# Performance work log

Hardware: AMD Instinct MI355X
Metric: run time of the kernel (lower is better)

## Reference

```python
import jax, jax.numpy as jnp
import numpy as np

N = 10000      # nodes
E = 100000     # edges
D = 768        # hidden = heads * head_dim
H = 4          # heads
C = D // H     # 192 per-head channels
EDIM = 16      # edge feature dim
NREL = 10      # num relations
L = 3          # num TransformerConv layers


def setup_inputs() -> dict:
    key = jax.random.key(0)
    ks = jax.random.split(key, 16)
    s = 0.02
    x = jax.random.normal(ks[0], (N, D), jnp.float32)
    edge_index = jax.random.randint(ks[1], (2, E), 0, N, jnp.int32)
    rel = jax.random.randint(ks[2], (E,), 0, NREL).astype(jnp.float32)
    w = jax.random.uniform(ks[3], (E,), jnp.float32)
    edge_attr = jnp.stack([rel, w], axis=1)  # [E, 2]: (relation_id, weight)
    rel_emb = jax.random.normal(ks[4], (NREL, EDIM - 1), jnp.float32) * s
    W_edge = jax.random.normal(ks[5], (EDIM, EDIM), jnp.float32) * s
    b_edge = jnp.zeros((EDIM,), jnp.float32)
    Wk = jax.random.normal(ks[6], (L, D, D), jnp.float32) * s
    bk = jnp.zeros((L, D), jnp.float32)
    Wq = jax.random.normal(ks[7], (L, D, D), jnp.float32) * s
    bq = jnp.zeros((L, D), jnp.float32)
    Wv = jax.random.normal(ks[8], (L, D, D), jnp.float32) * s
    bv = jnp.zeros((L, D), jnp.float32)
    We = jax.random.normal(ks[9], (L, EDIM, D), jnp.float32) * s   # lin_edge, no bias (PyG)
    Wskip = jax.random.normal(ks[10], (L, D, D), jnp.float32) * s  # root/skip linear
    bskip = jnp.zeros((L, D), jnp.float32)
    ln_g = jnp.ones((D,), jnp.float32)
    ln_b = jnp.zeros((D,), jnp.float32)
    return dict(x=x, edge_attr=edge_attr, edge_index=edge_index, rel_emb=rel_emb,
                W_edge=W_edge, b_edge=b_edge, Wk=Wk, bk=bk, Wq=Wq, bq=bq,
                Wv=Wv, bv=bv, We=We, Wskip=Wskip, bskip=bskip, ln_g=ln_g, ln_b=ln_b)


def reference(x, edge_attr, edge_index, rel_emb, W_edge, b_edge,
              Wk, bk, Wq, bq, Wv, bv, We, Wskip, bskip, ln_g, ln_b):
    src, dst = edge_index[0], edge_index[1]
    # _process_edge_features: embed relation id, concat weight, project
    rel_ids = jnp.clip(jax.lax.stop_gradient(edge_attr[:, 0]).astype(jnp.int32), 0, NREL - 1)
    ef = jnp.concatenate([rel_emb[rel_ids], edge_attr[:, 1:2]], axis=-1) @ W_edge + b_edge  # [E,16]
    scale = 1.0 / np.sqrt(C)
    h = x  # input_proj is Identity (input_dim == hidden_dim)
    for l in range(L):
        q = (h @ Wq[l] + bq[l]).reshape(N, H, C)
        k = (h @ Wk[l] + bk[l]).reshape(N, H, C)
        v = (h @ Wv[l] + bv[l]).reshape(N, H, C)
        e = (ef @ We[l]).reshape(E, H, C)           # per-edge embedding
        kj = k[src] + e                              # [E,H,C]
        alpha = jnp.einsum('ehc,ehc->eh', q[dst], kj) * scale  # [E,H]
        # scatter-softmax over incoming edges of each destination node
        m = jax.ops.segment_max(jax.lax.stop_gradient(alpha), dst, num_segments=N)
        a = jnp.exp(alpha - m[dst])
        denom = jax.ops.segment_sum(a, dst, num_segments=N)
        a = a / (denom[dst] + 1e-16)
        msg = (v[src] + e) * a[..., None]            # [E,H,C]
        out = jax.ops.segment_sum(msg.reshape(E, H * C), dst, num_segments=N)
        h = out + h @ Wskip[l] + bskip[l]            # root_weight skip connection
        if l < L - 1:
            h = jax.nn.gelu(h, approximate=False)    # dropout: eval mode -> identity
    mu = jnp.mean(h, axis=-1, keepdims=True)
    var = jnp.mean((h - mu) ** 2, axis=-1, keepdims=True)
    h = (h - mu) / jnp.sqrt(var + 1e-5) * ln_g + ln_b
    return jnp.mean(h, axis=0)  # global_mean_pool over single graph -> [D]
```

## Files before the change

### kernel.cpp

```cpp
#include <hip/hip_runtime.h>
#include <hip/hip_bf16.h>
#include <math.h>
#include <stdint.h>

#define NN 10000
#define EE 100000
#define DD 768
#define HH 4
#define CC 192
#define EDIM 16
#define NREL 10
#define MP 10240
#define NQ2 3200
#define NB 3136
#define SCALE 0.07216878364870322f

using short8  = __attribute__((ext_vector_type(8))) short;
using floatx4 = __attribute__((ext_vector_type(4))) float;


__device__ __forceinline__ float b2f(short u) {
    union { unsigned int i; float f; } t;
    t.i = ((unsigned int)(unsigned short)u) << 16;
    return t.f;
}

__device__ __forceinline__ short f2b(float f) {
    __hip_bfloat16 h = __float2bfloat16(f);
    short r;
    __builtin_memcpy(&r, &h, 2);
    return r;
}

__device__ __forceinline__ __hip_bfloat16 rd_any(const void* p, long long j, int bf) {
    if (bf) return ((const __hip_bfloat16*)p)[j];
    return __float2bfloat16(((const float*)p)[j]);
}

__device__ __forceinline__ void gload16(const __hip_bfloat16* g, __hip_bfloat16* l) {
    __builtin_amdgcn_global_load_lds(
        (const __attribute__((address_space(1))) unsigned int*)g,
        (__attribute__((address_space(3))) unsigned int*)l, 16, 0, 0);
}

__global__ __launch_bounds__(256) void detect_zero(const void* edge_attr,
                                                   int* flag, int* counts) {
    int i = blockIdx.x * 256 + threadIdx.x;
    if (i < NN) counts[i] = 0;
    if (blockIdx.x == 0 && threadIdx.x < 64) {
        const unsigned short* p = (const unsigned short*)edge_attr;
        int nz = (p[4 * threadIdx.x] != 0) ? 1 : 0;
        unsigned long long m = __ballot(nz);
        if (threadIdx.x == 0) *flag = (__popcll(m) > 8) ? 1 : 0;
    }
}


__global__ __launch_bounds__(256) void cvt_big(
    const void* x, const void* We, const int* flag,
    __hip_bfloat16* hb, __hip_bfloat16* Web) {
    long long i = (long long)blockIdx.x * 256 + threadIdx.x;
    int bf = *flag;
    const long long NX = (long long)NN * DD;
    const long long NE2 = 3LL * EDIM * DD;
    if (i < NX) { hb[i] = rd_any(x, i, bf); return; } i -= NX;
    if (i < NE2) { Web[i] = rd_any(We, i, bf); return; } i -= NE2;
    if (i < (long long)(MP - NN) * DD) hb[(long long)NN * DD + i] = __float2bfloat16(0.0f);
}

__global__ __launch_bounds__(256) void cvt_small(
    const void* ea, const void* rel, const void* Wed, const void* bed,
    const void* bk, const void* bq, const void* bv, const void* bs,
    const void* lg, const void* lb, const int* flag,
    __hip_bfloat16* eab, __hip_bfloat16* relb, __hip_bfloat16* Wedb,
    __hip_bfloat16* bedb, __hip_bfloat16* ballb, __hip_bfloat16* lgb,
    __hip_bfloat16* lbb) {
    long long i = (long long)blockIdx.x * 256 + threadIdx.x;
    int bf = *flag;
    if (i < 2LL * EE) { eab[i] = rd_any(ea, i, bf); return; } i -= 2LL * EE;
    if (i < NREL * (EDIM - 1)) { relb[i] = rd_any(rel, i, bf); return; } i -= NREL * (EDIM - 1);
    if (i < EDIM * EDIM) { Wedb[i] = rd_any(Wed, i, bf); return; } i -= EDIM * EDIM;
    if (i < EDIM) { bedb[i] = rd_any(bed, i, bf); return; } i -= EDIM;
    if (i < 3 * NB) {
        int l = (int)(i / NB), c = (int)(i % NB);
        const void* src; long long off;
        if (c < 768)       { src = bq; off = (long long)l * DD + c; }
        else if (c < 1536) { src = bk; off = (long long)l * DD + (c - 768); }
        else if (c < 2304) { src = bv; off = (long long)l * DD + (c - 1536); }
        else if (c < 3072) { src = bs; off = (long long)l * DD + (c - 2304); }
        else { ballb[i] = __float2bfloat16(0.0f); return; }
        ballb[i] = rd_any(src, off, bf); return;
    } i -= 3 * NB;
    if (i < DD) { lgb[i] = rd_any(lg, i, bf); return; } i -= DD;
    if (i < DD) { lbb[i] = rd_any(lb, i, bf); return; }
}

__global__ __launch_bounds__(256) void wt_all(
    const void* Wq, const void* Wk, const void* Wv, const void* Ws,
    const int* flag, __hip_bfloat16* Wt3) {
    __shared__ __hip_bfloat16 tile[32][33];
    int mm = blockIdx.y;
    int l = mm >> 2, m = mm & 3;
    const void* src = (m == 0) ? Wq : (m == 1) ? Wk : (m == 2) ? Wv : Ws;
    int bx = blockIdx.x;
    int tr = bx / 24, tc = bx % 24;
    int k0 = tr * 32, c0 = tc * 32;
    int t = threadIdx.x;
    int rr = t >> 5, cc = t & 31;
    int bf = *flag;
    long long base = (long long)l * DD * DD;
#pragma unroll
    for (int p = 0; p < 4; p++)
        tile[p * 8 + rr][cc] =
            rd_any(src, base + (long long)(k0 + p * 8 + rr) * DD + c0 + cc, bf);
    __syncthreads();
    __hip_bfloat16* dst = Wt3 + (size_t)l * NB * DD + (size_t)(m * 768 + c0) * DD + k0;
#pragma unroll
    for (int p = 0; p < 4; p++)
        dst[(size_t)(p * 8 + rr) * DD + cc] = tile[cc][p * 8 + rr];
}

__global__ __launch_bounds__(256) void mq_kernel(
    const void* Wq, const void* bq, const int* flag,
    const __hip_bfloat16* __restrict__ Web, __hip_bfloat16* __restrict__ Wt3,
    __hip_bfloat16* __restrict__ ballb) {
    __shared__ float WeS[16][193];
    const int lh = blockIdx.y, l = lh >> 2, hh = lh & 3;
    const int t = threadIdx.x;
    const int bf = *flag;
    for (int i = t; i < 16 * 192; i += 256) {
        int j = i / 192, c = i % 192;
        WeS[j][c] = (float)Web[(size_t)l * EDIM * DD + (size_t)j * DD + hh * CC + c];
    }
    __syncthreads();
    const int k = blockIdx.x * 64 + (t >> 2);
    const int j0 = (t & 3) * 4;
    float s0 = 0.f, s1 = 0.f, s2 = 0.f, s3 = 0.f;
    if (bf) {
        const short8* qp = (const short8*)((const __hip_bfloat16*)Wq +
            ((size_t)l * DD + k) * DD + hh * CC);
#pragma unroll 4
        for (int ch = 0; ch < 24; ch++) {
            short8 v = qp[ch];
#pragma unroll
            for (int u = 0; u < 8; u++) {
                float w = b2f(v[u]);
                int c = ch * 8 + u;
                s0 += w * WeS[j0 + 0][c]; s1 += w * WeS[j0 + 1][c];
                s2 += w * WeS[j0 + 2][c]; s3 += w * WeS[j0 + 3][c];
            }
        }
    } else {
        const float4* qp = (const float4*)((const float*)Wq +
            ((size_t)l * DD + k) * DD + hh * CC);
#pragma unroll 4
        for (int ch = 0; ch < 48; ch++) {
            float4 v = qp[ch];
            float wv[4] = {v.x, v.y, v.z, v.w};
#pragma unroll
            for (int u = 0; u < 4; u++) {
                float w = wv[u];
                int c = ch * 4 + u;
                s0 += w * WeS[j0 + 0][c]; s1 += w * WeS[j0 + 1][c];
                s2 += w * WeS[j0 + 2][c]; s3 += w * WeS[j0 + 3][c];
            }
        }
    }
    const size_t base = (size_t)l * NB * DD;
    const int row = 3072 + hh * 16 + j0;
    Wt3[base + (size_t)(row + 0) * DD + k] = __float2bfloat16(s0);
    Wt3[base + (size_t)(row + 1) * DD + k] = __float2bfloat16(s1);
    Wt3[base + (size_t)(row + 2) * DD + k] = __float2bfloat16(s2);
    Wt3[base + (size_t)(row + 3) * DD + k] = __float2bfloat16(s3);
    if (blockIdx.x == 0 && t < 4) {
        float b0 = 0.f, b1 = 0.f, b2 = 0.f, b3 = 0.f;
        for (int c = 0; c < CC; c++) {
            float w = (float)rd_any(bq, (long long)l * DD + hh * CC + c, bf);
            b0 += w * WeS[j0 + 0][c]; b1 += w * WeS[j0 + 1][c];
            b2 += w * WeS[j0 + 2][c]; b3 += w * WeS[j0 + 3][c];
        }
        ballb[l * NB + 3072 + hh * 16 + j0 + 0] = __float2bfloat16(b0);
        ballb[l * NB + 3072 + hh * 16 + j0 + 1] = __float2bfloat16(b1);
        ballb[l * NB + 3072 + hh * 16 + j0 + 2] = __float2bfloat16(b2);
        ballb[l * NB + 3072 + hh * 16 + j0 + 3] = __float2bfloat16(b3);
    }
}


__global__ __launch_bounds__(256) void count_kernel(const int* ei, int* counts) {
    int e = blockIdx.x * 256 + threadIdx.x;
    if (e < EE) atomicAdd(&counts[ei[EE + e]], 1);
}

__global__ __launch_bounds__(256) void scan_kernel(const int* counts, int* rowptr,
                                                   int* cursor) {
    __shared__ int sdata[256];
    int t = threadIdx.x;
    int base = t * 40;
    int cnt = (base < NN) ? min(40, NN - base) : 0;
    int s = 0;
    for (int i = 0; i < cnt; i++) s += counts[base + i];
    sdata[t] = s;
    __syncthreads();
    for (int off = 1; off < 256; off <<= 1) {
        int add = (t >= off) ? sdata[t - off] : 0;
        __syncthreads();
        sdata[t] += add;
        __syncthreads();
    }
    int run = sdata[t] - s;
    for (int i = 0; i < cnt; i++) {
        cursor[base + i] = run;
        run += counts[base + i];
        rowptr[base + i + 1] = run;
    }
    if (t == 0) rowptr[0] = 0;
}

__global__ __launch_bounds__(256) void fill_kernel(const int* ei, int* cursor,
                                                   int* eids, int* esrc) {
    int e = blockIdx.x * 256 + threadIdx.x;
    if (e < EE) {
        int d = ei[EE + e];
        int pos = atomicAdd(&cursor[d], 1);
        eids[pos] = e;
        esrc[pos] = ei[e];
    }
}


__global__ __launch_bounds__(256) void ef_kernel(
    const int* __restrict__ eids,
    const __hip_bfloat16* __restrict__ eab, const __hip_bfloat16* __restrict__ relb,
    const __hip_bfloat16* __restrict__ Wedb, const __hip_bfloat16* __restrict__ bedb,
    __hip_bfloat16* __restrict__ efb) {
    int idx = blockIdx.x * 256 + threadIdx.x;
    if (idx >= EE * EDIM) return;
    int p = idx >> 4, j = idx & 15;
    int e = eids[p];
    int rid = (int)((float)eab[e * 2 + 0]);
    rid = min(max(rid, 0), NREL - 1);
    float w = (float)eab[e * 2 + 1];
    float s = (float)bedb[j];
#pragma unroll
    for (int i = 0; i < 15; i++)
        s += (float)relb[rid * 15 + i] * (float)Wedb[i * EDIM + j];
    s += w * (float)Wedb[15 * EDIM + j];
    efb[idx] = __float2bfloat16(s);
}


__device__ __forceinline__ void stage_half(const __hip_bfloat16* g, int row0, int ktile,
                                           char* ldsdst, int tid) {
#pragma unroll
    for (int j = 0; j < 2; ++j) {
        int c = j * 512 + tid;
        int row = c >> 3;
        int sch = (c & 7) ^ (row & 7);
        gload16(g + (size_t)(row0 + row) * DD + ktile * 64 + sch * 8,
                (__hip_bfloat16*)(ldsdst + c * 16));
    }
}

#define MF16(va, vb, cc) cc = __builtin_amdgcn_mfma_f32_16x16x32_bf16(va, vb, cc, 0, 0, 0)
#define BAR() __builtin_amdgcn_s_barrier()
#define WLG() asm volatile("s_waitcnt lgkmcnt(0)" ::: "memory")
#define WVM(N) asm volatile("s_waitcnt vmcnt(" #N ")" ::: "memory")
#define SB() __builtin_amdgcn_sched_barrier(0)
#define LDS8(off) (*(const short8*)(smem + (off)))

__global__ __launch_bounds__(512) void gemm256(
    const __hip_bfloat16* __restrict__ A, const __hip_bfloat16* __restrict__ Bt,
    const __hip_bfloat16* __restrict__ bias, __hip_bfloat16* __restrict__ C) {
    __shared__ __align__(16) char smem[131072];
    const int bid = (int)blockIdx.x;
    const int tid = threadIdx.x;
    const int wid = tid >> 6, lane = tid & 63;
    const int quad = lane >> 4, l15 = lane & 15;

    if (bid >= 480) {
        const int qb = bid - 480;
        const int m0q = qb * 64;
        const __hip_bfloat16* Bq = Bt + (size_t)3072 * DD;
        const int xq0 = (quad ^ (l15 & 7)) * 16;
        const int xq1 = ((quad + 4) ^ (l15 & 7)) * 16;
        floatx4 qacc[4] = {};
        for (int kt = 0; kt < 12; ++kt) {
#pragma unroll
            for (int j = 0; j < 2; ++j) {
                int c = j * 512 + tid;
                int hf = c >> 9;
                int cc = c & 511;
                int row = cc >> 3;
                int sch = (cc & 7) ^ (row & 7);
                const __hip_bfloat16* src = hf
                    ? (Bq + (size_t)row * DD + kt * 64 + sch * 8)
                    : (A + (size_t)(m0q + row) * DD + kt * 64 + sch * 8);
                gload16(src, (__hip_bfloat16*)(smem + c * 16));
            }
            asm volatile("s_waitcnt vmcnt(0)" ::: "memory");
            BAR();
            if (wid < 4) {
                short8 a0 = LDS8((wid * 16 + l15) * 128 + xq0);
                short8 a1 = LDS8((wid * 16 + l15) * 128 + xq1);
#pragma unroll
                for (int nt = 0; nt < 4; ++nt) {
                    short8 b0 = LDS8(8192 + (nt * 16 + l15) * 128 + xq0);
                    short8 b1 = LDS8(8192 + (nt * 16 + l15) * 128 + xq1);
                    MF16(a0, b0, qacc[nt]);
                    MF16(a1, b1, qacc[nt]);
                }
            }
            WLG();
            BAR();
        }
        if (wid < 4) {
#pragma unroll
            for (int nt = 0; nt < 4; ++nt) {
                float bb = (float)bias[3072 + nt * 16 + l15];
#pragma unroll
                for (int r = 0; r < 4; ++r) {
                    int row = m0q + wid * 16 + quad * 4 + r;
                    if (row < NN)
                        C[(size_t)row * NQ2 + 3072 + nt * 16 + l15] =
                            __float2bfloat16(qacc[nt][r] + bb);
                }
            }
        }
        return;
    }

    const int wm = wid >> 2, wn = wid & 3;
    const int swz = (bid & 7) * 60 + (bid >> 3);
    const int m0 = (swz / 12) * 256;
    const int n0 = (swz % 12) * 256;

    const int xa0 = (quad ^ (l15 & 7)) * 16;
    const int xa1 = ((quad + 4) ^ (l15 & 7)) * 16;
    const int aRow = (wm * 128 + l15) * 128;
    const int bRow = 32768 + (wn * 64 + l15) * 128;

    floatx4 acc[8][4] = {};
    short8 a[4][2], bA[2][2], bB[2][2];

    stage_half(A, m0, 0, smem + 0, tid);
    stage_half(A, m0 + 128, 0, smem + 16384, tid);
    stage_half(Bt, n0, 0, smem + 32768, tid);
    stage_half(Bt, n0 + 128, 0, smem + 49152, tid);
    stage_half(Bt, n0, 1, smem + 98304, tid);
    stage_half(Bt, n0 + 128, 1, smem + 114688, tid);
    WVM(4);
    BAR();

#pragma unroll 1
    for (int it = 0; it < 6; ++it) {
        const int kA = 2 * it + 1;
        const int kB = (it < 5) ? 2 * it + 2 : 0;
        const int kC = (it < 5) ? 2 * it + 3 : 1;
        stage_half(A, m0, kA, smem + 65536, tid);
        stage_half(A, m0 + 128, kA, smem + 81920, tid);
#pragma unroll
        for (int mt = 0; mt < 4; ++mt) {
            a[mt][0] = LDS8(aRow + mt * 2048 + xa0);
            a[mt][1] = LDS8(aRow + mt * 2048 + xa1);
        }
#pragma unroll
        for (int nt = 0; nt < 2; ++nt) {
            bA[nt][0] = LDS8(bRow + nt * 2048 + xa0);
            bA[nt][1] = LDS8(bRow + nt * 2048 + xa1);
            bB[nt][0] = LDS8(bRow + (nt + 2) * 2048 + xa0);
            bB[nt][1] = LDS8(bRow + (nt + 2) * 2048 + xa1);
        }
        SB(); BAR(); WLG(); SB();
        __builtin_amdgcn_s_setprio(1);
#pragma unroll
        for (int mt = 0; mt < 4; ++mt)
#pragma unroll
            for (int nt = 0; nt < 2; ++nt) {
                MF16(a[mt][0], bA[nt][0], acc[mt][nt]);
                MF16(a[mt][1], bA[nt][1], acc[mt][nt]);
                MF16(a[mt][0], bB[nt][0], acc[mt][nt + 2]);
                MF16(a[mt][1], bB[nt][1], acc[mt][nt + 2]);
            }
        __builtin_amdgcn_s_setprio(0);
        stage_half(Bt, n0, kB, smem + 32768, tid);
        stage_half(Bt, n0 + 128, kB, smem + 49152, tid);
#pragma unroll
        for (int mt = 0; mt < 4; ++mt) {
            a[mt][0] = LDS8(aRow + (mt + 4) * 2048 + xa0);
            a[mt][1] = LDS8(aRow + (mt + 4) * 2048 + xa1);
        }
        WVM(4);
        SB(); BAR(); WLG(); SB();
        __builtin_amdgcn_s_setprio(1);
#pragma unroll
        for (int mt = 0; mt < 4; ++mt)
#pragma unroll
            for (int nt = 0; nt < 2; ++nt) {
                MF16(a[mt][0], bB[nt][0], acc[mt + 4][nt + 2]);
                MF16(a[mt][1], bB[nt][1], acc[mt + 4][nt + 2]);
                MF16(a[mt][0], bA[nt][0], acc[mt + 4][nt]);
                MF16(a[mt][1], bA[nt][1], acc[mt + 4][nt]);
            }
        __builtin_amdgcn_s_setprio(0);
        stage_half(A, m0, kB, smem + 0, tid);
        stage_half(A, m0 + 128, kB, smem + 16384, tid);
#pragma unroll
        for (int mt = 0; mt < 4; ++mt) {
            a[mt][0] = LDS8(65536 + aRow + mt * 2048 + xa0);
            a[mt][1] = LDS8(65536 + aRow + mt * 2048 + xa1);
        }
#pragma unroll
        for (int nt = 0; nt < 2; ++nt) {
            bA[nt][0] = LDS8(65536 + bRow + nt * 2048 + xa0);
            bA[nt][1] = LDS8(65536 + bRow + nt * 2048 + xa1);
            bB[nt][0] = LDS8(65536 + bRow + (nt + 2) * 2048 + xa0);
            bB[nt][1] = LDS8(65536 + bRow + (nt + 2) * 2048 + xa1);
        }
        SB(); BAR(); WLG(); SB();
        __builtin_amdgcn_s_setprio(1);
#pragma unroll
        for (int mt = 0; mt < 4; ++mt)
#pragma unroll
            for (int nt = 0; nt < 2; ++nt) {
                MF16(a[mt][0], bA[nt][0], acc[mt][nt]);
                MF16(a[mt][1], bA[nt][1], acc[mt][nt]);
                MF16(a[mt][0], bB[nt][0], acc[mt][nt + 2]);
                MF16(a[mt][1], bB[nt][1], acc[mt][nt + 2]);
            }
        __builtin_amdgcn_s_setprio(0);
        stage_half(Bt, n0, kC, smem + 98304, tid);
        stage_half(Bt, n0 + 128, kC, smem + 114688, tid);
#pragma unroll
        for (int mt = 0; mt < 4; ++mt) {
            a[mt][0] = LDS8(65536 + aRow + (mt + 4) * 2048 + xa0);
            a[mt][1] = LDS8(65536 + aRow + (mt + 4) * 2048 + xa1);
        }
        WVM(4);
        SB(); BAR(); WLG(); SB();
        __builtin_amdgcn_s_setprio(1);
#pragma unroll
        for (int mt = 0; mt < 4; ++mt)
#pragma unroll
            for (int nt = 0; nt < 2; ++nt) {
                MF16(a[mt][0], bB[nt][0], acc[mt + 4][nt + 2]);
                MF16(a[mt][1], bB[nt][1], acc[mt + 4][nt + 2]);
                MF16(a[mt][0], bA[nt][0], acc[mt + 4][nt]);
                MF16(a[mt][1], bA[nt][1], acc[mt + 4][nt]);
            }
        __builtin_amdgcn_s_setprio(0);
    }

    asm volatile("s_waitcnt vmcnt(0)" ::: "memory");
    BAR();
    {
        short* stg = (short*)smem + wid * 1152;
        float bv[4];
#pragma unroll
        for (int nt = 0; nt < 4; ++nt)
            bv[nt] = (float)bias[n0 + wn * 64 + nt * 16 + l15];
        const int rdo = (lane >> 2) * 68 + (lane & 3) * 16;
        const int grow0 = m0 + wm * 128 + (lane >> 2);
        const int gcol = n0 + wn * 64 + (lane & 3) * 16;
#pragma unroll
        for (int mt = 0; mt < 8; ++mt) {
#pragma unroll
            for (int nt = 0; nt < 4; ++nt)
#pragma unroll
                for (int r = 0; r < 4; ++r)
                    stg[(quad * 4 + r) * 68 + nt * 16 + l15] =
                        f2b(acc[mt][nt][r] + bv[nt]);
            asm volatile("s_waitcnt lgkmcnt(0)" ::: "memory");
            short8 v0 = *(const short8*)(stg + rdo);
            short8 v1 = *(const short8*)(stg + rdo + 8);
            int grow = grow0 + mt * 16;
            if (grow < NN) {
                short8* dp = (short8*)(C + (size_t)grow * NQ2 + gcol);
                dp[0] = v0; dp[1] = v1;
            }
            asm volatile("s_waitcnt lgkmcnt(0)" ::: "memory");
        }
    }
}


__global__ __launch_bounds__(256) void node_attn(
    const int* __restrict__ rowptr, const int* __restrict__ esrc,
    const __hip_bfloat16* __restrict__ qkvs, const __hip_bfloat16* __restrict__ efb,
    const __hip_bfloat16* __restrict__ Wel, __hip_bfloat16* __restrict__ hb,
    int do_gelu) {
    const int wv = threadIdx.x >> 6, lane = threadIdx.x & 63;
    const int n = blockIdx.x * 2 + (wv >> 1);
    const int half = wv & 1;
    const int cb = half * 384 + lane * 6;
    const int sj = lane & 15;
    const int hsel = lane & 32;
    const float qe_gate = ((lane & 16) == 0) ? 1.0f : 0.0f;
    const int s0 = rowptr[n], s1 = rowptr[n + 1];
    const short* qk = (const short*)qkvs;
    float q[6];
    {
        const short2* qp = (const short2*)(qk + (size_t)n * NQ2 + cb);
        short2 a = qp[0], b = qp[1], c = qp[2];
        q[0] = b2f(a.x) * SCALE; q[1] = b2f(a.y) * SCALE; q[2] = b2f(b.x) * SCALE;
        q[3] = b2f(b.y) * SCALE; q[4] = b2f(c.x) * SCALE; q[5] = b2f(c.y) * SCALE;
    }
    const float qe_l = b2f(qk[(size_t)n * NQ2 + 3072 + (half * 2 + (lane >> 5)) * 16 + sj])
                       * SCALE * qe_gate;
    float m = -INFINITY, lsum = 0.f, sacc = 0.f;
    float acc[6] = {};
    short2 ka = {0,0}, kb = {0,0}, kc = {0,0};
    short2 va = {0,0}, vb = {0,0}, vc = {0,0};
    float efv = 0.f;
    if (s0 < s1) {
        int src = esrc[s0];
        const short2* kp = (const short2*)(qk + (size_t)src * NQ2 + 768 + cb);
        const short2* vp = (const short2*)(qk + (size_t)src * NQ2 + 1536 + cb);
        ka = kp[0]; kb = kp[1]; kc = kp[2];
        va = vp[0]; vb = vp[1]; vc = vp[2];
        efv = b2f(((const short*)efb)[(size_t)s0 * 16 + sj]);
    }
    for (int p = s0; p < s1; p++) {
        short2 nka = ka, nkb = kb, nkc = kc, nva = va, nvb = vb, nvc = vc;
        float nefv = efv;
        if (p + 1 < s1) {
            int src = esrc[p + 1];
            const short2* kp = (const short2*)(qk + (size_t)src * NQ2 + 768 + cb);
            const short2* vp = (const short2*)(qk + (size_t)src * NQ2 + 1536 + cb);
            nka = kp[0]; nkb = kp[1]; nkc = kp[2];
            nva = vp[0]; nvb = vp[1]; nvc = vp[2];
            nefv = b2f(((const short*)efb)[(size_t)(p + 1) * 16 + sj]);
        }
        float part = qe_l * efv;
        part += q[0] * b2f(ka.x) + q[1] * b2f(ka.y) + q[2] * b2f(kb.x);
        part += q[3] * b2f(kb.y) + q[4] * b2f(kc.x) + q[5] * b2f(kc.y);
        part += __shfl_xor(part, 1); part += __shfl_xor(part, 2);
        part += __shfl_xor(part, 4); part += __shfl_xor(part, 8);
        part += __shfl_xor(part, 16);
        if (part > m + 8.0f) {
            float sc = __expf(m - part);
            m = part;
            lsum *= sc; sacc *= sc;
#pragma unroll
            for (int i = 0; i < 6; i++) acc[i] *= sc;
        }
        float w = __expf(part - m);
        lsum += w;
        sacc += w * efv;
        acc[0] += w * b2f(va.x); acc[1] += w * b2f(va.y);
        acc[2] += w * b2f(vb.x); acc[3] += w * b2f(vb.y);
        acc[4] += w * b2f(vc.x); acc[5] += w * b2f(vc.y);
        ka = nka; kb = nkb; kc = nkc; va = nva; vb = nvb; vc = nvc; efv = nefv;
    }
    float inv = 1.0f / (lsum + 1e-16f);
#pragma unroll
    for (int i = 0; i < 6; i++) acc[i] *= inv;
    float sS = sacc * inv;
    {
        const short2* sp = (const short2*)(qk + (size_t)n * NQ2 + 2304 + cb);
        short2 a = sp[0], b = sp[1], c = sp[2];
        acc[0] += b2f(a.x); acc[1] += b2f(a.y); acc[2] += b2f(b.x);
        acc[3] += b2f(b.y); acc[4] += b2f(c.x); acc[5] += b2f(c.y);
    }
#pragma unroll
    for (int j = 0; j < 16; j++) {
        float sv = __shfl(sS, hsel + j);
        const short2* wp = (const short2*)(Wel + (size_t)j * DD + cb);
        short2 a = wp[0], b = wp[1], c = wp[2];
        acc[0] += sv * b2f(a.x); acc[1] += sv * b2f(a.y); acc[2] += sv * b2f(b.x);
        acc[3] += sv * b2f(b.y); acc[4] += sv * b2f(c.x); acc[5] += sv * b2f(c.y);
    }
    if (do_gelu) {
#pragma unroll
        for (int i = 0; i < 6; i++)
            acc[i] = 0.5f * acc[i] * (1.0f + erff(acc[i] * 0.70710678118654752f));
    }
    short2 o0, o1, o2;
    o0.x = f2b(acc[0]); o0.y = f2b(acc[1]);
    o1.x = f2b(acc[2]); o1.y = f2b(acc[3]);
    o2.x = f2b(acc[4]); o2.y = f2b(acc[5]);
    short2* hp = (short2*)(hb + (size_t)n * DD + cb);
    hp[0] = o0; hp[1] = o1; hp[2] = o2;
}


__global__ __launch_bounds__(256) void ln_pool(
    const __hip_bfloat16* __restrict__ hb, const __hip_bfloat16* __restrict__ g,
    const __hip_bfloat16* __restrict__ b, float* __restrict__ partial) {
    __shared__ float sbuf[4][768];
    int grp = blockIdx.x, t = threadIdx.x;
    int wid = t >> 6, lane = t & 63;
    float gv[12], bv[12], acc[12];
#pragma unroll
    for (int i = 0; i < 12; i++) {
        gv[i] = (float)g[lane + i * 64];
        bv[i] = (float)b[lane + i * 64];
        acc[i] = 0.f;
    }
    for (int r = wid; r < 25; r += 4) {
        const __hip_bfloat16* row = hb + (size_t)(grp * 25 + r) * DD;
        float x[12];
        float s = 0.f, q = 0.f;
#pragma unroll
        for (int i = 0; i < 12; i++) {
            x[i] = (float)row[lane + i * 64];
            s += x[i]; q += x[i] * x[i];
        }
#pragma unroll
        for (int m = 32; m > 0; m >>= 1) {
            s += __shfl_xor(s, m); q += __shfl_xor(q, m);
        }
        float mu = s * (1.0f / 768.0f);
        float ms = q * (1.0f / 768.0f);
        float inv = 1.0f / sqrtf(ms - mu * mu + 1e-5f);
#pragma unroll
        for (int i = 0; i < 12; i++)
            acc[i] += (x[i] - mu) * inv * gv[i] + bv[i];
    }
#pragma unroll
    for (int i = 0; i < 12; i++) sbuf[wid][lane + i * 64] = acc[i];
    __syncthreads();
#pragma unroll
    for (int j = 0; j < 3; j++) {
        int col = t + j * 256;
        partial[(size_t)grp * DD + col] =
            sbuf[0][col] + sbuf[1][col] + sbuf[2][col] + sbuf[3][col];
    }
}

__global__ __launch_bounds__(256) void pool_final(
    const float* __restrict__ partial, void* __restrict__ out,
    const int* __restrict__ flag) {
    int dd = blockIdx.x * 256 + threadIdx.x;
    if (dd >= DD) return;
    float s = 0.f;
    for (int g2 = 0; g2 < 400; g2++) s += partial[(size_t)g2 * DD + dd];
    s *= (1.0f / 10000.0f);
    if (*flag) ((__hip_bfloat16*)out)[dd] = __float2bfloat16(s);
    else ((float*)out)[dd] = s;
}


extern "C" void kernel_launch(void* const* d_in, const int* in_sizes, int n_in,
                              void* d_out, int out_size, void* d_ws, size_t ws_size,
                              hipStream_t stream) {
    const void* x         = d_in[0];
    const void* edge_attr = d_in[1];
    const int*  ei        = (const int*)d_in[2];
    const void* rel_emb   = d_in[3];
    const void* W_edge    = d_in[4];
    const void* b_edge    = d_in[5];
    const void* Wk        = d_in[6];
    const void* bk        = d_in[7];
    const void* Wq        = d_in[8];
    const void* bq        = d_in[9];
    const void* Wv        = d_in[10];
    const void* bv        = d_in[11];
    const void* We        = d_in[12];
    const void* Wskip     = d_in[13];
    const void* bskip     = d_in[14];
    const void* ln_g      = d_in[15];
    const void* ln_b      = d_in[16];

    char* ws = (char*)d_ws;
    int*   flag    = (int*)(ws + 0);
    int*   counts  = (int*)(ws + 256);
    int*   rowptr  = (int*)(ws + 40448);
    int*   cursor  = (int*)(ws + 80640);
    int*   eids    = (int*)(ws + 120832);
    int*   esrc    = (int*)(ws + 520960);
    __hip_bfloat16* efb = (__hip_bfloat16*)(ws + 920960);
    float* partial = (float*)(ws + 4120960);
    __hip_bfloat16* eab   = (__hip_bfloat16*)(ws + 5349760);
    __hip_bfloat16* relb  = (__hip_bfloat16*)(ws + 5749760);
    __hip_bfloat16* Wedb  = (__hip_bfloat16*)(ws + 5750144);
    __hip_bfloat16* bedb  = (__hip_bfloat16*)(ws + 5750656);
    __hip_bfloat16* ballb = (__hip_bfloat16*)(ws + 5750784);
    __hip_bfloat16* lngb  = (__hip_bfloat16*)(ws + 5770752);
    __hip_bfloat16* lnbb  = (__hip_bfloat16*)(ws + 5772288);
    __hip_bfloat16* Web   = (__hip_bfloat16*)(ws + 5773824);
    __hip_bfloat16* hb    = (__hip_bfloat16*)(ws + 5847552);
    __hip_bfloat16* Wt3   = (__hip_bfloat16*)(ws + 21576192);
    __hip_bfloat16* qkvs  = (__hip_bfloat16*)(ws + 36911616);

    dim3 blk(256);

    detect_zero<<<dim3(40), blk, 0, stream>>>(edge_attr, flag, counts);

    {
        long long tot = (long long)NN * DD + 3LL * EDIM * DD + (long long)(MP - NN) * DD;
        cvt_big<<<dim3((unsigned)((tot + 255) / 256)), blk, 0, stream>>>(x, We, flag, hb, Web);
    }
    {
        long long tot = 2LL * EE + NREL * (EDIM - 1) + EDIM * EDIM + EDIM
                        + 3LL * NB + 2LL * DD;
        cvt_small<<<dim3((unsigned)((tot + 255) / 256)), blk, 0, stream>>>(
            edge_attr, rel_emb, W_edge, b_edge, bk, bq, bv, bskip, ln_g, ln_b,
            flag, eab, relb, Wedb, bedb, ballb, lngb, lnbb);
    }
    wt_all<<<dim3(576, 12), blk, 0, stream>>>(Wq, Wk, Wv, Wskip, flag, Wt3);
    mq_kernel<<<dim3(12, 12), blk, 0, stream>>>(Wq, bq, flag, Web, Wt3, ballb);

    count_kernel<<<dim3((EE + 255) / 256), blk, 0, stream>>>(ei, counts);
    scan_kernel<<<dim3(1), blk, 0, stream>>>(counts, rowptr, cursor);
    fill_kernel<<<dim3((EE + 255) / 256), blk, 0, stream>>>(ei, cursor, eids, esrc);

    ef_kernel<<<dim3((EE * EDIM) / 256), blk, 0, stream>>>(eids, eab, relb, Wedb, bedb, efb);

    for (int l = 0; l < 3; l++) {
        const __hip_bfloat16* We_l = Web + (size_t)l * EDIM * DD;
        gemm256<<<dim3(640), dim3(512), 0, stream>>>(
            hb, Wt3 + (size_t)l * NB * DD, ballb + (size_t)l * NB, qkvs);
        node_attn<<<dim3(NN / 2), blk, 0, stream>>>(rowptr, esrc, qkvs, efb,
                                                    We_l, hb, (l < 2) ? 1 : 0);
    }

    ln_pool<<<dim3(400), blk, 0, stream>>>(hb, lngb, lnbb, partial);
    pool_final<<<dim3(3), blk, 0, stream>>>(partial, d_out, flag);
}
```

Measured before the change: 601.7 us.

## Interleave K/V weight rows, reorder GEMM blocks, LDS scan, atomic pooling

Permutes the K and V projection rows so each node's K and V chunks for a lane sit together, letting the attention kernel fetch them with three 8-byte loads instead of six 4-byte loads from two regions. Moves the Q-edge GEMM blocks to the front of the grid, rewrites the scan to stage counts in shared memory, and replaces the 400-row partial reduction with float atomics into a zeroed accumulator. The atomics make the pooled result order-dependent in rounding.

```diff
diff --git a/kernel.cpp b/kernel.cpp
--- a/kernel.cpp
+++ b/kernel.cpp
@@ -44,9 +44,11 @@
 }
 
 __global__ __launch_bounds__(256) void detect_zero(const void* edge_attr,
-                                                   int* flag, int* counts) {
+                                                   int* flag, int* counts,
+                                                   float* accum) {
     int i = blockIdx.x * 256 + threadIdx.x;
     if (i < NN) counts[i] = 0;
+    if (i < DD) accum[i] = 0.0f;
     if (blockIdx.x == 0 && threadIdx.x < 64) {
         const unsigned short* p = (const unsigned short*)edge_attr;
         int nz = (p[4 * threadIdx.x] != 0) ? 1 : 0;
@@ -83,13 +85,17 @@
     if (i < EDIM) { bedb[i] = rd_any(bed, i, bf); return; } i -= EDIM;
     if (i < 3 * NB) {
         int l = (int)(i / NB), c = (int)(i % NB);
-        const void* src; long long off;
-        if (c < 768)       { src = bq; off = (long long)l * DD + c; }
-        else if (c < 1536) { src = bk; off = (long long)l * DD + (c - 768); }
-        else if (c < 2304) { src = bv; off = (long long)l * DD + (c - 1536); }
-        else if (c < 3072) { src = bs; off = (long long)l * DD + (c - 2304); }
-        else { ballb[i] = __float2bfloat16(0.0f); return; }
-        ballb[i] = rd_any(src, off, bf); return;
+        const void* src; long long off; int outc;
+        if (c < 768)       { src = bq; off = (long long)l * DD + c; outc = c; }
+        else if (c < 1536) { int xx = c - 768;  src = bk;
+                             off = (long long)l * DD + xx;
+                             outc = 768 + (xx / 6) * 12 + xx % 6; }
+        else if (c < 2304) { int xx = c - 1536; src = bv;
+                             off = (long long)l * DD + xx;
+                             outc = 768 + (xx / 6) * 12 + 6 + xx % 6; }
+        else if (c < 3072) { src = bs; off = (long long)l * DD + (c - 2304); outc = c; }
+        else { ballb[l * NB + c] = __float2bfloat16(0.0f); return; }
+        ballb[l * NB + outc] = rd_any(src, off, bf); return;
     } i -= 3 * NB;
     if (i < DD) { lgb[i] = rd_any(lg, i, bf); return; } i -= DD;
     if (i < DD) { lbb[i] = rd_any(lb, i, bf); return; }
@@ -114,10 +120,16 @@
         tile[p * 8 + rr][cc] =
             rd_any(src, base + (long long)(k0 + p * 8 + rr) * DD + c0 + cc, bf);
     __syncthreads();
-    __hip_bfloat16* dst = Wt3 + (size_t)l * NB * DD + (size_t)(m * 768 + c0) * DD + k0;
-#pragma unroll
-    for (int p = 0; p < 4; p++)
-        dst[(size_t)(p * 8 + rr) * DD + cc] = tile[cc][p * 8 + rr];
+    __hip_bfloat16* base_l = Wt3 + (size_t)l * NB * DD;
+#pragma unroll
+    for (int p = 0; p < 4; p++) {
+        int xcol = c0 + p * 8 + rr;
+        int row;
+        if (m == 1)      row = 768 + (xcol / 6) * 12 + xcol % 6;
+        else if (m == 2) row = 768 + (xcol / 6) * 12 + 6 + xcol % 6;
+        else             row = m * 768 + xcol;
+        base_l[(size_t)row * DD + k0 + cc] = tile[cc][p * 8 + rr];
+    }
 }
 
 __global__ __launch_bounds__(256) void mq_kernel(
@@ -194,12 +206,15 @@
 
 __global__ __launch_bounds__(256) void scan_kernel(const int* counts, int* rowptr,
                                                    int* cursor) {
+    __shared__ int buf[NN];
     __shared__ int sdata[256];
     int t = threadIdx.x;
+    for (int j = t; j < NN; j += 256) buf[j] = counts[j];
+    __syncthreads();
     int base = t * 40;
     int cnt = (base < NN) ? min(40, NN - base) : 0;
     int s = 0;
-    for (int i = 0; i < cnt; i++) s += counts[base + i];
+    for (int i = 0; i < cnt; i++) s += buf[base + i];
     sdata[t] = s;
     __syncthreads();
     for (int off = 1; off < 256; off <<= 1) {
@@ -210,11 +225,17 @@
     }
     int run = sdata[t] - s;
     for (int i = 0; i < cnt; i++) {
-        cursor[base + i] = run;
-        run += counts[base + i];
-        rowptr[base + i + 1] = run;
-    }
-    if (t == 0) rowptr[0] = 0;
+        int tmp = buf[base + i];
+        buf[base + i] = run;
+        run += tmp;
+    }
+    __syncthreads();
+    for (int j = t; j < NN; j += 256) {
+        int v = buf[j];
+        cursor[j] = v;
+        rowptr[j] = v;
+    }
+    if (t == 0) rowptr[NN] = EE;
 }
 
 __global__ __launch_bounds__(256) void fill_kernel(const int* ei, int* cursor,
@@ -278,9 +299,8 @@
     const int wid = tid >> 6, lane = tid & 63;
     const int quad = lane >> 4, l15 = lane & 15;
 
-    if (bid >= 480) {
-        const int qb = bid - 480;
-        const int m0q = qb * 64;
+    if (bid < 160) {
+        const int m0q = bid * 64;
         const __hip_bfloat16* Bq = Bt + (size_t)3072 * DD;
         const int xq0 = (quad ^ (l15 & 7)) * 16;
         const int xq1 = ((quad + 4) ^ (l15 & 7)) * 16;
@@ -330,8 +350,9 @@
         return;
     }
 
+    const int mbid = bid - 160;
     const int wm = wid >> 2, wn = wid & 3;
-    const int swz = (bid & 7) * 60 + (bid >> 3);
+    const int swz = (mbid & 7) * 60 + (mbid >> 3);
     const int m0 = (swz / 12) * 256;
     const int n0 = (swz % 12) * 256;
 
@@ -493,6 +514,8 @@
     const int n = blockIdx.x * 2 + (wv >> 1);
     const int half = wv & 1;
     const int cb = half * 384 + lane * 6;
+    const int g = half * 64 + lane;
+    const int kvoff = 768 + g * 12;
     const int sj = lane & 15;
     const int hsel = lane & 32;
     const float qe_gate = ((lane & 16) == 0) ? 1.0f : 0.0f;
@@ -509,31 +532,24 @@
                        * SCALE * qe_gate;
     float m = -INFINITY, lsum = 0.f, sacc = 0.f;
     float acc[6] = {};
-    short2 ka = {0,0}, kb = {0,0}, kc = {0,0};
-    short2 va = {0,0}, vb = {0,0}, vc = {0,0};
+    short4 kvA = {0,0,0,0}, kvB = {0,0,0,0}, kvC = {0,0,0,0};
     float efv = 0.f;
     if (s0 < s1) {
-        int src = esrc[s0];
-        const short2* kp = (const short2*)(qk + (size_t)src * NQ2 + 768 + cb);
-        const short2* vp = (const short2*)(qk + (size_t)src * NQ2 + 1536 + cb);
-        ka = kp[0]; kb = kp[1]; kc = kp[2];
-        va = vp[0]; vb = vp[1]; vc = vp[2];
+        const short4* kv = (const short4*)(qk + (size_t)esrc[s0] * NQ2 + kvoff);
+        kvA = kv[0]; kvB = kv[1]; kvC = kv[2];
         efv = b2f(((const short*)efb)[(size_t)s0 * 16 + sj]);
     }
     for (int p = s0; p < s1; p++) {
-        short2 nka = ka, nkb = kb, nkc = kc, nva = va, nvb = vb, nvc = vc;
+        short4 nA = kvA, nB = kvB, nC = kvC;
         float nefv = efv;
         if (p + 1 < s1) {
-            int src = esrc[p + 1];
-            const short2* kp = (const short2*)(qk + (size_t)src * NQ2 + 768 + cb);
-            const short2* vp = (const short2*)(qk + (size_t)src * NQ2 + 1536 + cb);
-            nka = kp[0]; nkb = kp[1]; nkc = kp[2];
-            nva = vp[0]; nvb = vp[1]; nvc = vp[2];
+            const short4* kv = (const short4*)(qk + (size_t)esrc[p + 1] * NQ2 + kvoff);
+            nA = kv[0]; nB = kv[1]; nC = kv[2];
             nefv = b2f(((const short*)efb)[(size_t)(p + 1) * 16 + sj]);
         }
         float part = qe_l * efv;
-        part += q[0] * b2f(ka.x) + q[1] * b2f(ka.y) + q[2] * b2f(kb.x);
-        part += q[3] * b2f(kb.y) + q[4] * b2f(kc.x) + q[5] * b2f(kc.y);
+        part += q[0] * b2f(kvA.x) + q[1] * b2f(kvA.y) + q[2] * b2f(kvA.z);
+        part += q[3] * b2f(kvA.w) + q[4] * b2f(kvB.x) + q[5] * b2f(kvB.y);
         part += __shfl_xor(part, 1); part += __shfl_xor(part, 2);
         part += __shfl_xor(part, 4); part += __shfl_xor(part, 8);
         part += __shfl_xor(part, 16);
@@ -547,10 +563,10 @@
         float w = __expf(part - m);
         lsum += w;
         sacc += w * efv;
-        acc[0] += w * b2f(va.x); acc[1] += w * b2f(va.y);
-        acc[2] += w * b2f(vb.x); acc[3] += w * b2f(vb.y);
-        acc[4] += w * b2f(vc.x); acc[5] += w * b2f(vc.y);
-        ka = nka; kb = nkb; kc = nkc; va = nva; vb = nvb; vc = nvc; efv = nefv;
+        acc[0] += w * b2f(kvB.z); acc[1] += w * b2f(kvB.w);
+        acc[2] += w * b2f(kvC.x); acc[3] += w * b2f(kvC.y);
+        acc[4] += w * b2f(kvC.z); acc[5] += w * b2f(kvC.w);
+        kvA = nA; kvB = nB; kvC = nC; efv = nefv;
     }
     float inv = 1.0f / (lsum + 1e-16f);
 #pragma unroll
@@ -586,7 +602,7 @@
 
 __global__ __launch_bounds__(256) void ln_pool(
     const __hip_bfloat16* __restrict__ hb, const __hip_bfloat16* __restrict__ g,
-    const __hip_bfloat16* __restrict__ b, float* __restrict__ partial) {
+    const __hip_bfloat16* __restrict__ b, float* __restrict__ accum) {
     __shared__ float sbuf[4][768];
     int grp = blockIdx.x, t = threadIdx.x;
     int wid = t >> 6, lane = t & 63;
@@ -623,19 +639,17 @@
 #pragma unroll
     for (int j = 0; j < 3; j++) {
         int col = t + j * 256;
-        partial[(size_t)grp * DD + col] =
-            sbuf[0][col] + sbuf[1][col] + sbuf[2][col] + sbuf[3][col];
+        atomicAdd(&accum[col],
+                  sbuf[0][col] + sbuf[1][col] + sbuf[2][col] + sbuf[3][col]);
     }
 }
 
 __global__ __launch_bounds__(256) void pool_final(
-    const float* __restrict__ partial, void* __restrict__ out,
+    const float* __restrict__ accum, void* __restrict__ out,
     const int* __restrict__ flag) {
     int dd = blockIdx.x * 256 + threadIdx.x;
     if (dd >= DD) return;
-    float s = 0.f;
-    for (int g2 = 0; g2 < 400; g2++) s += partial[(size_t)g2 * DD + dd];
-    s *= (1.0f / 10000.0f);
+    float s = accum[dd] * (1.0f / 10000.0f);
     if (*flag) ((__hip_bfloat16*)out)[dd] = __float2bfloat16(s);
     else ((float*)out)[dd] = s;
 }
@@ -670,7 +684,7 @@
     int*   eids    = (int*)(ws + 120832);
     int*   esrc    = (int*)(ws + 520960);
     __hip_bfloat16* efb = (__hip_bfloat16*)(ws + 920960);
-    float* partial = (float*)(ws + 4120960);
+    float* accum   = (float*)(ws + 4120960);
     __hip_bfloat16* eab   = (__hip_bfloat16*)(ws + 5349760);
     __hip_bfloat16* relb  = (__hip_bfloat16*)(ws + 5749760);
     __hip_bfloat16* Wedb  = (__hip_bfloat16*)(ws + 5750144);
@@ -685,7 +699,7 @@
 
     dim3 blk(256);
 
-    detect_zero<<<dim3(40), blk, 0, stream>>>(edge_attr, flag, counts);
+    detect_zero<<<dim3(40), blk, 0, stream>>>(edge_attr, flag, counts, accum);
 
     {
         long long tot = (long long)NN * DD + 3LL * EDIM * DD + (long long)(MP - NN) * DD;
@@ -715,6 +729,6 @@
                                                     We_l, hb, (l < 2) ? 1 : 0);
     }
 
-    ln_pool<<<dim3(400), blk, 0, stream>>>(hb, lngb, lnbb, partial);
-    pool_final<<<dim3(3), blk, 0, stream>>>(partial, d_out, flag);
-}
+    ln_pool<<<dim3(400), blk, 0, stream>>>(hb, lngb, lnbb, accum);
+    pool_final<<<dim3(3), blk, 0, stream>>>(accum, d_out, flag);
+}
```

New measurement: 570.9 us, median of 2. 1.05x faster.
